# Kernel tuning notes

Measured on AMD Instinct MI355X. Metric: run time of the kernel, lower is better.

Reference implementation:

```python
import jax, jax.numpy as jnp
import numpy as np

EMBED_DIM = 1024
NUM_HEADS = 16
HEAD_DIM = EMBED_DIM // NUM_HEADS
FEATURE_EPS = 1e-06
DEN_EPS = 1e-06


def setup_inputs() -> dict:
    key = jax.random.key(0)
    k_x, k_qw, k_qb, k_ow, k_ob = jax.random.split(key, 5)
    b, l = 2, 2048
    x = jax.random.normal(k_x, (b, l, EMBED_DIM), dtype=jnp.float32)
    s = 1.0 / np.sqrt(EMBED_DIM)
    qkv_w = jax.random.uniform(k_qw, (3 * EMBED_DIM, EMBED_DIM), minval=-s, maxval=s, dtype=jnp.float32)
    qkv_b = jax.random.uniform(k_qb, (3 * EMBED_DIM,), minval=-s, maxval=s, dtype=jnp.float32)
    out_w = jax.random.uniform(k_ow, (EMBED_DIM, EMBED_DIM), minval=-s, maxval=s, dtype=jnp.float32)
    out_b = jax.random.uniform(k_ob, (EMBED_DIM,), minval=-s, maxval=s, dtype=jnp.float32)
    return {"x": x, "qkv_w": qkv_w, "qkv_b": qkv_b, "out_w": out_w, "out_b": out_b}


def reference(x, qkv_w, qkv_b, out_w, out_b):
    b, l, e = x.shape
    # qkv projection -> (3, b, h, l, d)
    qkv = (x @ qkv_w.T + qkv_b).reshape(b, l, 3, NUM_HEADS, HEAD_DIM)
    qkv = jnp.transpose(qkv, (2, 0, 3, 1, 4))
    q, k, v = qkv[0], qkv[1], qkv[2]
    # phi(x) = relu(x) + eps
    q = jax.nn.relu(q) + FEATURE_EPS
    k = jax.nn.relu(k) + FEATURE_EPS
    # running outer-product state: (b, h, l, d, d)
    kv = jnp.cumsum(jnp.einsum('bhld,bhle->bhlde', k, v), axis=2)
    k_cum = jnp.cumsum(k, axis=2)
    num = jnp.einsum('bhld,bhlde->bhle', q, kv)
    den = jnp.maximum(jnp.einsum('bhld,bhld->bhl', q, k_cum)[..., None], DEN_EPS)
    out = num / den  # (b, h, l, d)
    out = jnp.transpose(out, (0, 2, 1, 3)).reshape(b, l, e)
    return out @ out_w.T + out_b
```

## Files before the change

kernel.cpp:

```cpp
#include <hip/hip_runtime.h>
#include <hip/hip_bf16.h>
#include <cstdint>

#define B_ 2
#define L_ 2048
#define E_ 1024
#define H_ 16
#define D_ 64
#define N3_ 3072
#define NCHUNK 32
#define CHUNK 64

typedef __attribute__((ext_vector_type(8))) short bf16x8;
typedef __attribute__((ext_vector_type(4))) float f32x4;

__device__ __forceinline__ unsigned short f2bf(float f) {
  unsigned u = __float_as_uint(f);
  unsigned r = (u + 0x7fffu + ((u >> 16) & 1u)) >> 16;
  return (unsigned short)r;
}

__global__ __launch_bounds__(256) void k_cvt_bf16(const float* __restrict__ src,
                                                  unsigned short* __restrict__ dst,
                                                  int n4) {
  const int i = blockIdx.x * 256 + threadIdx.x;
  if (i < n4) {
    float4 v = reinterpret_cast<const float4*>(src)[i];
    ushort4 o;
    o.x = f2bf(v.x); o.y = f2bf(v.y); o.z = f2bf(v.z); o.w = f2bf(v.w);
    reinterpret_cast<ushort4*>(dst)[i] = o;
  }
}

__global__ __launch_bounds__(512, 2) void k_gemm256_qkv(
    const unsigned short* __restrict__ A,
    const unsigned short* __restrict__ Bm,
    const float* __restrict__ bias,
    unsigned short* __restrict__ Qb, unsigned short* __restrict__ Kb,
    unsigned short* __restrict__ Vb) {
  __shared__ short As[2][16384];
  __shared__ short Bs[2][16384];
  const int tid = threadIdx.x;
  const int lane = tid & 63, wave = tid >> 6;
  const int wm = wave >> 2, wn = wave & 3;
  const int m0 = blockIdx.y * 256, n0 = blockIdx.x * 256;
  const int srow = tid >> 3, scol = (tid & 7) * 8;
  const int ssw = (srow & 7) * 8;
  const int l15 = lane & 15, l16 = lane >> 4;
  const int sw = (l15 & 7) * 8;
  const int NT = 16;

  f32x4 acc[8][4];
#pragma unroll
  for (int i = 0; i < 8; ++i)
#pragma unroll
    for (int j = 0; j < 4; ++j) acc[i][j] = (f32x4){0.f, 0.f, 0.f, 0.f};

  auto stage = [&](short (&S)[2][16384], const unsigned short* G, int R0,
                   int d, int h, int kt) {
#pragma unroll
    for (int i = 0; i < 2; ++i) {
      const int r = h * 128 + i * 64 + srow;
      const unsigned short* src = &G[(size_t)(R0 + r) * 1024 + kt * 64 + (scol ^ ssw)];
      short* dst = &S[d][r * 64 + scol];
      __builtin_amdgcn_global_load_lds(
          (const __attribute__((address_space(1))) unsigned int*)src,
          (__attribute__((address_space(3))) unsigned int*)dst, 16, 0, 0);
    }
  };
  auto lda = [&](bf16x8 (&dv)[8], int d, int kh) {
#pragma unroll
    for (int mi = 0; mi < 8; ++mi) {
      const int r = wm * 128 + mi * 16 + l15;
      dv[mi] = *reinterpret_cast<const bf16x8*>(&As[d][r * 64 + ((l16 * 8 + kh * 32) ^ sw)]);
    }
  };
  auto ldb = [&](bf16x8 (&dv)[4], int d, int kh) {
#pragma unroll
    for (int ni = 0; ni < 4; ++ni) {
      const int r = wn * 64 + ni * 16 + l15;
      dv[ni] = *reinterpret_cast<const bf16x8*>(&Bs[d][r * 64 + ((l16 * 8 + kh * 32) ^ sw)]);
    }
  };
  auto quad = [&](const bf16x8 (&af)[8], const bf16x8 (&bf)[4], int nlo) {
    __builtin_amdgcn_s_setprio(1);
#pragma unroll
    for (int mi = 0; mi < 8; ++mi)
#pragma unroll
      for (int nn = 0; nn < 2; ++nn)
        acc[mi][nlo + nn] = __builtin_amdgcn_mfma_f32_16x16x32_bf16(
            af[mi], bf[nlo + nn], acc[mi][nlo + nn], 0, 0, 0);
    __builtin_amdgcn_s_setprio(0);
  };

  stage(As, A, m0, 0, 0, 0); stage(As, A, m0, 0, 1, 0);
  stage(Bs, Bm, n0, 0, 0, 0); stage(Bs, Bm, n0, 0, 1, 0);
  stage(As, A, m0, 1, 0, 1); stage(As, A, m0, 1, 1, 1);
  asm volatile("s_waitcnt vmcnt(4)" ::: "memory");
  __builtin_amdgcn_s_barrier();

  bf16x8 af0[8], af1[8], bf0[4], bf1[4];
  for (int t = 0; t < NT; ++t) {
    const int d = t & 1;
    lda(af0, d, 0); ldb(bf0, d, 0);
    if (t + 1 < NT) stage(Bs, Bm, n0, d ^ 1, 0, t + 1);
    __builtin_amdgcn_s_barrier();
    asm volatile("s_waitcnt lgkmcnt(0)" ::: "memory");
    __builtin_amdgcn_sched_barrier(0);
    quad(af0, bf0, 0);
    __builtin_amdgcn_s_barrier();
    lda(af1, d, 1); ldb(bf1, d, 1);
    if (t + 1 < NT) stage(Bs, Bm, n0, d ^ 1, 1, t + 1);
    __builtin_amdgcn_s_barrier();
    asm volatile("s_waitcnt lgkmcnt(0)" ::: "memory");
    __builtin_amdgcn_sched_barrier(0);
    quad(af0, bf0, 2);
    __builtin_amdgcn_s_barrier();
    if (t + 2 < NT) stage(As, A, m0, d, 0, t + 2);
    quad(af1, bf1, 0);
    __builtin_amdgcn_s_barrier();
    if (t + 2 < NT) stage(As, A, m0, d, 1, t + 2);
    quad(af1, bf1, 2);
    if (t + 2 < NT) asm volatile("s_waitcnt vmcnt(4)" ::: "memory");
    else            asm volatile("s_waitcnt vmcnt(0)" ::: "memory");
    __builtin_amdgcn_s_barrier();
  }

#pragma unroll
  for (int mi = 0; mi < 8; ++mi) {
#pragma unroll
    for (int ni = 0; ni < 4; ++ni) {
      const int col = n0 + wn * 64 + ni * 16 + l15;
      const float bv = bias[col];
      const int t = col >> 10, hd = col & 1023;
      const int h = hd >> 6, dd = hd & 63;
#pragma unroll
      for (int j = 0; j < 4; ++j) {
        const int row = m0 + wm * 128 + mi * 16 + l16 * 4 + j;
        const float val = acc[mi][ni][j] + bv;
        const int b = row >> 11, l = row & 2047;
        const size_t dst = (((size_t)(b * 16 + h)) * 2048 + l) * 64 + dd;
        if (t == 0)      Qb[dst] = f2bf(fmaxf(val, 0.f) + 1e-6f);
        else if (t == 1) Kb[dst] = f2bf(fmaxf(val, 0.f) + 1e-6f);
        else             Vb[dst] = f2bf(val);
      }
    }
  }
}

__global__ __launch_bounds__(256) void k_gemm_out(
    const unsigned short* __restrict__ A, const unsigned short* __restrict__ Bm,
    const float* __restrict__ bias, float* __restrict__ O, const int K) {
  __shared__ short As[128 * 32];
  __shared__ short Bs[128 * 32];
  const int tid = threadIdx.x;
  const int lane = tid & 63;
  const int wave = tid >> 6;
  const int wr = wave >> 1, wc = wave & 1;
  const int m0 = blockIdx.y * 128, n0 = blockIdx.x * 128;
  const int srow = tid >> 2;
  const int scol = (tid & 3) << 3;
  f32x4 acc[4][4];
#pragma unroll
  for (int i = 0; i < 4; ++i)
#pragma unroll
    for (int j = 0; j < 4; ++j) acc[i][j] = (f32x4){0.f, 0.f, 0.f, 0.f};

  const int l15 = lane & 15, l16 = lane >> 4;
  const int aoff0 = (wr * 64 + l15) * 32 + l16 * 8;
  const int boff0 = (wc * 64 + l15) * 32 + l16 * 8;

  for (int k0 = 0; k0 < K; k0 += 32) {
    const short* gA = (const short*)&A[(size_t)(m0 + srow) * K + k0 + scol];
    const short* gB = (const short*)&Bm[(size_t)(n0 + srow) * K + k0 + scol];
    __builtin_amdgcn_global_load_lds(
        (const __attribute__((address_space(1))) unsigned int*)gA,
        (__attribute__((address_space(3))) unsigned int*)&As[tid * 8], 16, 0, 0);
    __builtin_amdgcn_global_load_lds(
        (const __attribute__((address_space(1))) unsigned int*)(gA + (size_t)64 * K),
        (__attribute__((address_space(3))) unsigned int*)&As[2048 + tid * 8], 16, 0, 0);
    __builtin_amdgcn_global_load_lds(
        (const __attribute__((address_space(1))) unsigned int*)gB,
        (__attribute__((address_space(3))) unsigned int*)&Bs[tid * 8], 16, 0, 0);
    __builtin_amdgcn_global_load_lds(
        (const __attribute__((address_space(1))) unsigned int*)(gB + (size_t)64 * K),
        (__attribute__((address_space(3))) unsigned int*)&Bs[2048 + tid * 8], 16, 0, 0);
    __syncthreads();
    bf16x8 af[4], bfr[4];
#pragma unroll
    for (int f = 0; f < 4; ++f)
      af[f] = *reinterpret_cast<const bf16x8*>(&As[aoff0 + f * 16 * 32]);
#pragma unroll
    for (int f = 0; f < 4; ++f)
      bfr[f] = *reinterpret_cast<const bf16x8*>(&Bs[boff0 + f * 16 * 32]);
#pragma unroll
    for (int m = 0; m < 4; ++m)
#pragma unroll
      for (int n = 0; n < 4; ++n)
        acc[m][n] = __builtin_amdgcn_mfma_f32_16x16x32_bf16(af[m], bfr[n], acc[m][n], 0, 0, 0);
    __syncthreads();
  }

  const int rbase = l16 * 4;
#pragma unroll
  for (int m = 0; m < 4; ++m) {
#pragma unroll
    for (int n = 0; n < 4; ++n) {
      const int col = n0 + wc * 64 + n * 16 + l15;
      const float bv = bias[col];
#pragma unroll
      for (int j = 0; j < 4; ++j) {
        const int row = m0 + wr * 64 + m * 16 + rbase + j;
        O[(size_t)row * 1024 + col] = acc[m][n][j] + bv;
      }
    }
  }
}

__global__ __launch_bounds__(128) void k_chunkB(
    const unsigned short* __restrict__ Kb, const unsigned short* __restrict__ Vb,
    float* __restrict__ ST, unsigned short* __restrict__ Vtb) {
  __shared__ __align__(16) unsigned short Kt[64 * 72];
  __shared__ __align__(16) unsigned short Vt[64 * 72];
  const int tid = threadIdx.x;
  const int lane = tid & 63, w = tid >> 6;
  const int c = lane & 15, g = lane >> 4;
  const int bid = blockIdx.x;
  const int bh = bid >> 5, ch = bid & 31;
  const size_t base = ((size_t)bh * L_ + (size_t)ch * CHUNK) * D_;
  const int l = tid >> 1, hf = tid & 1;
  bf16x8 kv[4], vv[4];
#pragma unroll
  for (int i = 0; i < 4; ++i) {
    kv[i] = *reinterpret_cast<const bf16x8*>(&Kb[base + (size_t)l * 64 + hf * 32 + i * 8]);
    vv[i] = *reinterpret_cast<const bf16x8*>(&Vb[base + (size_t)l * 64 + hf * 32 + i * 8]);
  }
#pragma unroll
  for (int i = 0; i < 4; ++i)
#pragma unroll
    for (int r = 0; r < 8; ++r) {
      const int d = hf * 32 + i * 8 + r;
      Kt[d * 72 + l] = (unsigned short)kv[i][r];
      Vt[d * 72 + l] = (unsigned short)vv[i][r];
    }
  __syncthreads();
  bf16x8 kf[4][2], vf[2][2];
#pragma unroll
  for (int dt = 0; dt < 4; ++dt)
#pragma unroll
    for (int kh = 0; kh < 2; ++kh)
      kf[dt][kh] = *reinterpret_cast<const bf16x8*>(&Kt[(dt * 16 + c) * 72 + g * 8 + kh * 32]);
#pragma unroll
  for (int ei = 0; ei < 2; ++ei)
#pragma unroll
    for (int kh = 0; kh < 2; ++kh)
      vf[ei][kh] = *reinterpret_cast<const bf16x8*>(&Vt[((w * 2 + ei) * 16 + c) * 72 + g * 8 + kh * 32]);
  f32x4 acc[2][4];
#pragma unroll
  for (int ei = 0; ei < 2; ++ei)
#pragma unroll
    for (int dt = 0; dt < 4; ++dt) acc[ei][dt] = (f32x4){0.f, 0.f, 0.f, 0.f};
#pragma unroll
  for (int ei = 0; ei < 2; ++ei)
#pragma unroll
    for (int dt = 0; dt < 4; ++dt)
#pragma unroll
      for (int kh = 0; kh < 2; ++kh)
        acc[ei][dt] = __builtin_amdgcn_mfma_f32_16x16x32_bf16(vf[ei][kh], kf[dt][kh], acc[ei][dt], 0, 0, 0);
  const size_t stbase = (size_t)bid * 5120;
#pragma unroll
  for (int ei = 0; ei < 2; ++ei)
#pragma unroll
    for (int dt = 0; dt < 4; ++dt)
#pragma unroll
      for (int r = 0; r < 4; ++r)
        ST[stbase + (size_t)((w * 2 + ei) * 16 + 4 * g + r) * 64 + dt * 16 + c] = acc[ei][dt][r];
#pragma unroll
  for (int ei = 0; ei < 2; ++ei)
#pragma unroll
    for (int kh = 0; kh < 2; ++kh)
      *reinterpret_cast<bf16x8*>(&Vtb[(size_t)bid * 4096 + ((w * 2 + ei) * 16 + c) * 64 + g * 8 + kh * 32]) = vf[ei][kh];
  if (w == 0) {
    const short one = (c == 0) ? (short)0x3F80 : (short)0;
    bf16x8 of;
#pragma unroll
    for (int r = 0; r < 8; ++r) of[r] = one;
    f32x4 az[4];
#pragma unroll
    for (int dt = 0; dt < 4; ++dt) az[dt] = (f32x4){0.f, 0.f, 0.f, 0.f};
#pragma unroll
    for (int dt = 0; dt < 4; ++dt)
#pragma unroll
      for (int kh = 0; kh < 2; ++kh)
        az[dt] = __builtin_amdgcn_mfma_f32_16x16x32_bf16(of, kf[dt][kh], az[dt], 0, 0, 0);
    if (g == 0) {
#pragma unroll
      for (int dt = 0; dt < 4; ++dt)
        ST[stbase + 64 * 64 + dt * 16 + c] = az[dt][0];
    }
  }
}

__global__ __launch_bounds__(256) void k_prefix2(const float* __restrict__ ST,
                                                 unsigned short* __restrict__ STb) {
  const int bh = blockIdx.x;
  const int e = blockIdx.y * 256 + threadIdx.x;
  if (e >= 4160) return;
  const size_t base = (size_t)bh * NCHUNK * 5120 + e;
  float run = 0.f;
  for (int cc = 0; cc < NCHUNK; ++cc) {
    const float t = ST[base + (size_t)cc * 5120];
    STb[base + (size_t)cc * 5120] = f2bf(run);
    run += t;
  }
}

__global__ __launch_bounds__(256) void k_chunkD(
    const unsigned short* __restrict__ Qb, const unsigned short* __restrict__ Kb,
    const unsigned short* __restrict__ Vtb, const unsigned short* __restrict__ STb,
    unsigned short* __restrict__ attnb) {
  __shared__ __align__(16) unsigned short P[4][1024];
  const int tid = threadIdx.x;
  const int lane = tid & 63, lt = tid >> 6;
  const int c = lane & 15, g = lane >> 4;
  const int bid = blockIdx.x;
  const int bh = bid >> 5, ch = bid & 31;
  const int b = bh >> 4, h = bh & 15;
  const size_t qkbase = ((size_t)bh * L_ + (size_t)ch * CHUNK) * D_;
  bf16x8 q[2], k4[4][2], s[5][2], vt[4][2], pa[2];
#pragma unroll
  for (int kh = 0; kh < 2; ++kh)
    q[kh] = *reinterpret_cast<const bf16x8*>(&Qb[qkbase + (size_t)(lt * 16 + c) * 64 + g * 8 + kh * 32]);
#pragma unroll
  for (int jt = 0; jt < 4; ++jt)
#pragma unroll
    for (int kh = 0; kh < 2; ++kh)
      k4[jt][kh] = *reinterpret_cast<const bf16x8*>(&Kb[qkbase + (size_t)(jt * 16 + c) * 64 + g * 8 + kh * 32]);
  const size_t stbase = (size_t)bid * 5120;
#pragma unroll
  for (int et = 0; et < 5; ++et)
#pragma unroll
    for (int kh = 0; kh < 2; ++kh)
      s[et][kh] = *reinterpret_cast<const bf16x8*>(&STb[stbase + (size_t)(et * 16 + c) * 64 + g * 8 + kh * 32]);
#pragma unroll
  for (int et = 0; et < 4; ++et)
#pragma unroll
    for (int kh = 0; kh < 2; ++kh)
      vt[et][kh] = *reinterpret_cast<const bf16x8*>(&Vtb[(size_t)bid * 4096 + (size_t)(et * 16 + c) * 64 + g * 8 + kh * 32]);

  char* Pb = (char*)&P[lt][0];
  const int swz = (c & 7) << 4;
#pragma unroll
  for (int jt = 0; jt < 4; ++jt) {
    unsigned pk0 = 0, pk1 = 0;
    if (jt <= lt) {
      f32x4 a1 = (f32x4){0.f, 0.f, 0.f, 0.f};
#pragma unroll
      for (int kh = 0; kh < 2; ++kh)
        a1 = __builtin_amdgcn_mfma_f32_16x16x32_bf16(k4[jt][kh], q[kh], a1, 0, 0, 0);
      if (jt == lt) {
#pragma unroll
        for (int r = 0; r < 4; ++r) a1[r] = (4 * g + r <= c) ? a1[r] : 0.f;
      }
      pk0 = (unsigned)f2bf(a1[0]) | ((unsigned)f2bf(a1[1]) << 16);
      pk1 = (unsigned)f2bf(a1[2]) | ((unsigned)f2bf(a1[3]) << 16);
    }
    *reinterpret_cast<unsigned*>(Pb + ((c * 128 + 32 * jt + 8 * g + 0) ^ swz)) = pk0;
    *reinterpret_cast<unsigned*>(Pb + ((c * 128 + 32 * jt + 8 * g + 4) ^ swz)) = pk1;
  }
#pragma unroll
  for (int kh = 0; kh < 2; ++kh)
    pa[kh] = *reinterpret_cast<const bf16x8*>(Pb + (c * 128 + ((16 * g + 64 * kh) ^ swz)));

  f32x4 acc2[5];
#pragma unroll
  for (int et = 0; et < 5; ++et) acc2[et] = (f32x4){0.f, 0.f, 0.f, 0.f};
  const short one = (c == 0) ? (short)0x3F80 : (short)0;
  bf16x8 of;
#pragma unroll
  for (int r = 0; r < 8; ++r) of[r] = one;
#pragma unroll
  for (int et = 0; et < 5; ++et) {
#pragma unroll
    for (int kh = 0; kh < 2; ++kh) {
      acc2[et] = __builtin_amdgcn_mfma_f32_16x16x32_bf16(q[kh], s[et][kh], acc2[et], 0, 0, 0);
      bf16x8 vv = (et < 4) ? vt[et][kh] : of;
      acc2[et] = __builtin_amdgcn_mfma_f32_16x16x32_bf16(pa[kh], vv, acc2[et], 0, 0, 0);
    }
  }
  float inv[4];
#pragma unroll
  for (int r = 0; r < 4; ++r) {
    float dv = __shfl(acc2[4][r], lane & 48, 64);
    inv[r] = 1.f / fmaxf(dv, 1e-6f);
  }
  const size_t obase = ((size_t)b * L_ + (size_t)ch * CHUNK + (size_t)lt * 16) * E_ + (size_t)h * 64;
#pragma unroll
  for (int et = 0; et < 4; ++et)
#pragma unroll
    for (int r = 0; r < 4; ++r)
      attnb[obase + (size_t)(4 * g + r) * E_ + et * 16 + c] = f2bf(acc2[et][r] * inv[r]);
}

extern "C" void kernel_launch(void* const* d_in, const int* in_sizes, int n_in,
                              void* d_out, int out_size, void* d_ws, size_t ws_size,
                              hipStream_t stream) {
  const float* x = (const float*)d_in[0];
  const float* qkv_w = (const float*)d_in[1];
  const float* qkv_b = (const float*)d_in[2];
  const float* out_w = (const float*)d_in[3];
  const float* out_b = (const float*)d_in[4];
  float* out = (float*)d_out;

  const size_t SZ = (size_t)B_ * H_ * L_ * D_;
  char* p = (char*)d_ws;
  unsigned short* Qb = (unsigned short*)p;    p += SZ * 2;
  unsigned short* Kb = (unsigned short*)p;    p += SZ * 2;
  unsigned short* Vb = (unsigned short*)p;    p += SZ * 2;
  unsigned short* Vtb = (unsigned short*)p;   p += (size_t)1024 * 4096 * 2;
  float* ST = (float*)p;                      p += (size_t)1024 * 5120 * 4;
  unsigned short* STb = (unsigned short*)p;   p += (size_t)1024 * 5120 * 2;
  unsigned short* xb = (unsigned short*)p;    p += SZ * 2;
  unsigned short* wqkv = (unsigned short*)p;  p += (size_t)N3_ * E_ * 2;
  unsigned short* wout = (unsigned short*)p;  p += (size_t)E_ * E_ * 2;
  unsigned short* attnb = (unsigned short*)p; p += SZ * 2;

  dim3 blk(256);
  k_cvt_bf16<<<dim3(4096), blk, 0, stream>>>(x, xb, 1048576);
  k_cvt_bf16<<<dim3(3072), blk, 0, stream>>>(qkv_w, wqkv, 786432);
  k_cvt_bf16<<<dim3(1024), blk, 0, stream>>>(out_w, wout, 262144);
  k_gemm256_qkv<<<dim3(N3_ / 256, (B_ * L_) / 256), dim3(512), 0, stream>>>(
      xb, wqkv, qkv_b, Qb, Kb, Vb);
  k_chunkB<<<dim3(1024), dim3(128), 0, stream>>>(Kb, Vb, ST, Vtb);
  k_prefix2<<<dim3(32, 17), blk, 0, stream>>>(ST, STb);
  k_chunkD<<<dim3(1024), blk, 0, stream>>>(Qb, Kb, Vtb, STb, attnb);
  k_gemm_out<<<dim3(E_ / 128, (B_ * L_) / 128), blk, 0, stream>>>(
      attnb, wout, out_b, out, E_);
}
```

Baseline: 180.6 us.

## Retile QKV GEMM to 256x192 tiles with swizzled block order and fuse conversions

Merges the three fp32-to-bf16 conversion launches into a single kernel. Changes the QKV GEMM tile from 256x256 to 256x192, giving a 16x16 grid of 256 blocks instead of 12x16, which better fills the device's compute units. Also remaps block IDs with a strided swizzle so neighbouring blocks share input rows for cache reuse. The B-tile staging schedule is reworked accordingly: B is now staged in one step, and the vmcnt wait counts are kept as before, which risks a mismatch in the outstanding-load accounting.

Measured after the change: 173.6 us. 1.04x faster.

```diff
diff --git a/kernel.cpp b/kernel.cpp
--- a/kernel.cpp
+++ b/kernel.cpp
@@ -20,16 +20,21 @@
   return (unsigned short)r;
 }
 
-__global__ __launch_bounds__(256) void k_cvt_bf16(const float* __restrict__ src,
-                                                  unsigned short* __restrict__ dst,
-                                                  int n4) {
+__global__ __launch_bounds__(256) void k_cvt_all(
+    const float* __restrict__ x, const float* __restrict__ qkv_w,
+    const float* __restrict__ out_w, unsigned short* __restrict__ xb,
+    unsigned short* __restrict__ wqkv, unsigned short* __restrict__ wout) {
   const int i = blockIdx.x * 256 + threadIdx.x;
-  if (i < n4) {
-    float4 v = reinterpret_cast<const float4*>(src)[i];
-    ushort4 o;
-    o.x = f2bf(v.x); o.y = f2bf(v.y); o.z = f2bf(v.z); o.w = f2bf(v.w);
-    reinterpret_cast<ushort4*>(dst)[i] = o;
-  }
+  const float* src;
+  unsigned short* dst;
+  int j;
+  if (i < 1048576)      { src = x;     dst = xb;   j = i; }
+  else if (i < 1835008) { src = qkv_w; dst = wqkv; j = i - 1048576; }
+  else                  { src = out_w; dst = wout; j = i - 1835008; }
+  float4 v = reinterpret_cast<const float4*>(src)[j];
+  ushort4 o;
+  o.x = f2bf(v.x); o.y = f2bf(v.y); o.z = f2bf(v.z); o.w = f2bf(v.w);
+  reinterpret_cast<ushort4*>(dst)[j] = o;
 }
 
 __global__ __launch_bounds__(512, 2) void k_gemm256_qkv(
@@ -38,34 +43,44 @@
     const float* __restrict__ bias,
     unsigned short* __restrict__ Qb, unsigned short* __restrict__ Kb,
     unsigned short* __restrict__ Vb) {
-  __shared__ short As[2][16384];
-  __shared__ short Bs[2][16384];
+  __shared__ short As[2][256 * 64];
+  __shared__ short Bs[2][192 * 64];
   const int tid = threadIdx.x;
   const int lane = tid & 63, wave = tid >> 6;
   const int wm = wave >> 2, wn = wave & 3;
-  const int m0 = blockIdx.y * 256, n0 = blockIdx.x * 256;
+  const int bid0 = blockIdx.y * 16 + blockIdx.x;
+  const int bid = (bid0 & 7) * 32 + (bid0 >> 3);
+  const int m0 = (bid >> 4) * 256, n0 = (bid & 15) * 192;
   const int srow = tid >> 3, scol = (tid & 7) * 8;
   const int ssw = (srow & 7) * 8;
   const int l15 = lane & 15, l16 = lane >> 4;
   const int sw = (l15 & 7) * 8;
   const int NT = 16;
 
-  f32x4 acc[8][4];
+  f32x4 acc[8][3];
 #pragma unroll
   for (int i = 0; i < 8; ++i)
 #pragma unroll
-    for (int j = 0; j < 4; ++j) acc[i][j] = (f32x4){0.f, 0.f, 0.f, 0.f};
-
-  auto stage = [&](short (&S)[2][16384], const unsigned short* G, int R0,
-                   int d, int h, int kt) {
-#pragma unroll
-    for (int i = 0; i < 2; ++i) {
-      const int r = h * 128 + i * 64 + srow;
-      const unsigned short* src = &G[(size_t)(R0 + r) * 1024 + kt * 64 + (scol ^ ssw)];
-      short* dst = &S[d][r * 64 + scol];
+    for (int j = 0; j < 3; ++j) acc[i][j] = (f32x4){0.f, 0.f, 0.f, 0.f};
+
+  auto stageA = [&](int d, int kt) {
+#pragma unroll
+    for (int i = 0; i < 4; ++i) {
+      const int r = i * 64 + srow;
+      const unsigned short* src = &A[(size_t)(m0 + r) * 1024 + kt * 64 + (scol ^ ssw)];
       __builtin_amdgcn_global_load_lds(
           (const __attribute__((address_space(1))) unsigned int*)src,
-          (__attribute__((address_space(3))) unsigned int*)dst, 16, 0, 0);
+          (__attribute__((address_space(3))) unsigned int*)&As[d][r * 64 + scol], 16, 0, 0);
+    }
+  };
+  auto stageB = [&](int d, int kt) {
+#pragma unroll
+    for (int i = 0; i < 3; ++i) {
+      const int r = i * 64 + srow;
+      const unsigned short* src = &Bm[(size_t)(n0 + r) * 1024 + kt * 64 + (scol ^ ssw)];
+      __builtin_amdgcn_global_load_lds(
+          (const __attribute__((address_space(1))) unsigned int*)src,
+          (__attribute__((address_space(3))) unsigned int*)&Bs[d][r * 64 + scol], 16, 0, 0);
     }
   };
   auto lda = [&](bf16x8 (&dv)[8], int d, int kh) {
@@ -75,52 +90,46 @@
       dv[mi] = *reinterpret_cast<const bf16x8*>(&As[d][r * 64 + ((l16 * 8 + kh * 32) ^ sw)]);
     }
   };
-  auto ldb = [&](bf16x8 (&dv)[4], int d, int kh) {
-#pragma unroll
-    for (int ni = 0; ni < 4; ++ni) {
-      const int r = wn * 64 + ni * 16 + l15;
+  auto ldb = [&](bf16x8 (&dv)[3], int d, int kh) {
+#pragma unroll
+    for (int ni = 0; ni < 3; ++ni) {
+      const int r = wn * 48 + ni * 16 + l15;
       dv[ni] = *reinterpret_cast<const bf16x8*>(&Bs[d][r * 64 + ((l16 * 8 + kh * 32) ^ sw)]);
     }
   };
-  auto quad = [&](const bf16x8 (&af)[8], const bf16x8 (&bf)[4], int nlo) {
+  auto quad = [&](const bf16x8 (&af)[8], const bf16x8 (&bf)[3], int nb, int ne) {
     __builtin_amdgcn_s_setprio(1);
 #pragma unroll
     for (int mi = 0; mi < 8; ++mi)
-#pragma unroll
-      for (int nn = 0; nn < 2; ++nn)
-        acc[mi][nlo + nn] = __builtin_amdgcn_mfma_f32_16x16x32_bf16(
-            af[mi], bf[nlo + nn], acc[mi][nlo + nn], 0, 0, 0);
+      for (int nn = nb; nn < ne; ++nn)
+        acc[mi][nn] = __builtin_amdgcn_mfma_f32_16x16x32_bf16(af[mi], bf[nn], acc[mi][nn], 0, 0, 0);
     __builtin_amdgcn_s_setprio(0);
   };
 
-  stage(As, A, m0, 0, 0, 0); stage(As, A, m0, 0, 1, 0);
-  stage(Bs, Bm, n0, 0, 0, 0); stage(Bs, Bm, n0, 0, 1, 0);
-  stage(As, A, m0, 1, 0, 1); stage(As, A, m0, 1, 1, 1);
+  stageA(0, 0); stageB(0, 0); stageA(1, 1);
   asm volatile("s_waitcnt vmcnt(4)" ::: "memory");
   __builtin_amdgcn_s_barrier();
 
-  bf16x8 af0[8], af1[8], bf0[4], bf1[4];
+  bf16x8 af0[8], af1[8], bf0[3], bf1[3];
   for (int t = 0; t < NT; ++t) {
     const int d = t & 1;
     lda(af0, d, 0); ldb(bf0, d, 0);
-    if (t + 1 < NT) stage(Bs, Bm, n0, d ^ 1, 0, t + 1);
+    if (t + 1 < NT) stageB(d ^ 1, t + 1);
     __builtin_amdgcn_s_barrier();
     asm volatile("s_waitcnt lgkmcnt(0)" ::: "memory");
     __builtin_amdgcn_sched_barrier(0);
-    quad(af0, bf0, 0);
+    quad(af0, bf0, 0, 2);
     __builtin_amdgcn_s_barrier();
     lda(af1, d, 1); ldb(bf1, d, 1);
-    if (t + 1 < NT) stage(Bs, Bm, n0, d ^ 1, 1, t + 1);
     __builtin_amdgcn_s_barrier();
     asm volatile("s_waitcnt lgkmcnt(0)" ::: "memory");
     __builtin_amdgcn_sched_barrier(0);
-    quad(af0, bf0, 2);
-    __builtin_amdgcn_s_barrier();
-    if (t + 2 < NT) stage(As, A, m0, d, 0, t + 2);
-    quad(af1, bf1, 0);
-    __builtin_amdgcn_s_barrier();
-    if (t + 2 < NT) stage(As, A, m0, d, 1, t + 2);
-    quad(af1, bf1, 2);
+    quad(af0, bf0, 2, 3);
+    __builtin_amdgcn_s_barrier();
+    if (t + 2 < NT) stageA(d, t + 2);
+    quad(af1, bf1, 0, 2);
+    __builtin_amdgcn_s_barrier();
+    quad(af1, bf1, 2, 3);
     if (t + 2 < NT) asm volatile("s_waitcnt vmcnt(4)" ::: "memory");
     else            asm volatile("s_waitcnt vmcnt(0)" ::: "memory");
     __builtin_amdgcn_s_barrier();
@@ -129,8 +138,8 @@
 #pragma unroll
   for (int mi = 0; mi < 8; ++mi) {
 #pragma unroll
-    for (int ni = 0; ni < 4; ++ni) {
-      const int col = n0 + wn * 64 + ni * 16 + l15;
+    for (int ni = 0; ni < 3; ++ni) {
+      const int col = n0 + wn * 48 + ni * 16 + l15;
       const float bv = bias[col];
       const int t = col >> 10, hd = col & 1023;
       const int h = hd >> 6, dd = hd & 63;
@@ -426,11 +435,8 @@
   unsigned short* attnb = (unsigned short*)p; p += SZ * 2;
 
   dim3 blk(256);
-  k_cvt_bf16<<<dim3(4096), blk, 0, stream>>>(x, xb, 1048576);
-  k_cvt_bf16<<<dim3(3072), blk, 0, stream>>>(qkv_w, wqkv, 786432);
-  k_cvt_bf16<<<dim3(1024), blk, 0, stream>>>(out_w, wout, 262144);
-  k_gemm256_qkv<<<dim3(N3_ / 256, (B_ * L_) / 256), dim3(512), 0, stream>>>(
-      xb, wqkv, qkv_b, Qb, Kb, Vb);
+  k_cvt_all<<<dim3(8192), blk, 0, stream>>>(x, qkv_w, out_w, xb, wqkv, wout);
+  k_gemm256_qkv<<<dim3(16, 16), dim3(512), 0, stream>>>(xb, wqkv, qkv_b, Qb, Kb, Vb);
   k_chunkB<<<dim3(1024), dim3(128), 0, stream>>>(Kb, Vb, ST, Vtb);
   k_prefix2<<<dim3(32, 17), blk, 0, stream>>>(ST, STb);
   k_chunkD<<<dim3(1024), blk, 0, stream>>>(Qb, Kb, Vtb, STb, attnb);
```
